# Kernel tuning notes

Measured on AMD Instinct MI355X. Metric: run time of the kernel, lower is better.

Reference implementation:

```python
import jax, jax.numpy as jnp
import numpy as np

D_MODEL = 1024
H = 16
D_K = D_MODEL // H
B = 128   # batch (intersample attention attends across this dim)
N = 256   # samples / tokens per row


def setup_inputs() -> dict:
    key = jax.random.key(0)
    ks = jax.random.split(key, 8)
    s = 1.0 / np.sqrt(D_MODEL)
    return {
        "query": jax.random.normal(ks[0], (B, N, D_MODEL), jnp.float32),
        "key":   jax.random.normal(ks[1], (B, N, D_MODEL), jnp.float32),
        "value": jax.random.normal(ks[2], (B, N, D_MODEL), jnp.float32),
        "Wq": jax.random.normal(ks[3], (D_MODEL, D_MODEL), jnp.float32) * s,
        "bq": jnp.zeros((D_MODEL,), jnp.float32),
        "Wk": jax.random.normal(ks[4], (D_MODEL, D_MODEL), jnp.float32) * s,
        "bk": jnp.zeros((D_MODEL,), jnp.float32),
        "Wv": jax.random.normal(ks[5], (D_MODEL, D_MODEL), jnp.float32) * s,
        "bv": jnp.zeros((D_MODEL,), jnp.float32),
        "Wo": jax.random.normal(ks[6], (D_MODEL, D_MODEL), jnp.float32) * s,
        "bo": jnp.zeros((D_MODEL,), jnp.float32),
    }


def _proj_heads(x, W, b):
    # torch nn.Linear: x @ W.T + b ; then view (b, n, h, d_k) -> (b, h, n, d_k)
    y = jnp.einsum('bnd,ed->bne', x, W) + b
    bsz, n, _ = y.shape
    return y.reshape(bsz, n, H, D_K).transpose(0, 2, 1, 3)


def reference(query, key, value, Wq, bq, Wk, bk, Wv, bv, Wo, bo):
    q = _proj_heads(query, Wq, bq)  # (b, h, n, d_k)
    k = _proj_heads(key,   Wk, bk)
    v = _proj_heads(value, Wv, bv)
    # intersample attention: attend ACROSS the batch dim b (per head, per sample n)
    scale = 1.0 / jnp.sqrt(jnp.asarray(D_K, q.dtype))
    scores = jnp.einsum('bhnd,chnd->hnbc', q, k) * scale  # (h, n, b, b)
    p = jax.nn.softmax(scores, axis=-1)
    out = jnp.einsum('hnbc,chnd->bhnd', p, v)             # (b, h, n, d_k)
    # merge heads: (b, h, n, d_k) -> (b, n, h*d_k)
    bsz, _, n, _ = out.shape
    out = out.transpose(0, 2, 1, 3).reshape(bsz, n, H * D_K)
    return jnp.einsum('bnd,ed->bne', out, Wo) + bo
```

## Files before the change

### kernel.cpp

```cpp
#include <hip/hip_runtime.h>
#include <hip/hip_bf16.h>
#include <stdint.h>

#define D_MODEL 1024
#define HEADS   16
#define DK      64
#define BATCH   128
#define NTOK    256
#define MROWS   (BATCH * NTOK)

typedef __attribute__((ext_vector_type(8))) short bf16x8;
typedef __attribute__((ext_vector_type(4))) float f32x4;

__device__ __forceinline__ unsigned short f2b_rne(float f) {
    union { float f; unsigned int u; } c; c.f = f;
    unsigned int u = c.u;
    unsigned int r = (u + 0x7FFFu + ((u >> 16) & 1u)) >> 16;
    return (unsigned short)r;
}

__device__ __forceinline__ void async16(const void* g, void* l) {
    __builtin_amdgcn_global_load_lds(
        (__attribute__((address_space(1))) void*)g,
        (__attribute__((address_space(3))) void*)l,
        16, 0, 0);
}

__global__ __launch_bounds__(256)
void f2b_kernel(const float* __restrict__ x, ushort* __restrict__ y, int n4) {
    int i = blockIdx.x * blockDim.x + threadIdx.x;
    int stride = gridDim.x * blockDim.x;
    for (; i < n4; i += stride) {
        float4 v = ((const float4*)x)[i];
        ushort4 o;
        o.x = f2b_rne(v.x); o.y = f2b_rne(v.y);
        o.z = f2b_rne(v.z); o.w = f2b_rne(v.w);
        ((ushort4*)y)[i] = o;
    }
}

template<int MODE>
__global__ __launch_bounds__(256)
void gemm_nt(const ushort* __restrict__ A, const ushort* __restrict__ B,
             const float* __restrict__ bias, void* __restrict__ Cout,
             int M, int N, int K, float alpha)
{
    __shared__ ushort As[128 * 32];
    __shared__ ushort Bs[128 * 32];

    const int tid  = threadIdx.x;
    const int wave = tid >> 6, lane = tid & 63;
    const int quad = lane >> 4, l15 = lane & 15;
    const int pm = blockIdx.x * 128, pn = blockIdx.y * 128;
    const int wm = (wave & 1) * 64, wn = (wave >> 1) * 64;

    f32x4 acc[4][4] = {};

    const int rg = lane >> 2;
    const int c8 = (lane & 3) * 8;
    const ushort* Abase0 = A + (size_t)(pm + wave * 32 + rg) * K + c8;
    const ushort* Abase1 = Abase0 + (size_t)16 * K;
    const ushort* Bbase0 = B + (size_t)(pn + wave * 32 + rg) * K + c8;
    const ushort* Bbase1 = Bbase0 + (size_t)16 * K;

    for (int k0 = 0; k0 < K; k0 += 32) {
        __syncthreads();
        async16(Abase0 + k0, &As[wave * 1024]);
        async16(Abase1 + k0, &As[wave * 1024 + 512]);
        async16(Bbase0 + k0, &Bs[wave * 1024]);
        async16(Bbase1 + k0, &Bs[wave * 1024 + 512]);
        __syncthreads();

        bf16x8 af[4], bfr[4];
        #pragma unroll
        for (int t = 0; t < 4; t++) {
            af[t]  = *(const bf16x8*)&As[(wm + t * 16 + l15) * 32 + quad * 8];
            bfr[t] = *(const bf16x8*)&Bs[(wn + t * 16 + l15) * 32 + quad * 8];
        }
        #pragma unroll
        for (int i = 0; i < 4; i++)
            #pragma unroll
            for (int j = 0; j < 4; j++)
                acc[i][j] = __builtin_amdgcn_mfma_f32_16x16x32_bf16(af[i], bfr[j], acc[i][j], 0, 0, 0);
    }

    if (MODE == 0) {
        ushort* out = (ushort*)Cout;
        #pragma unroll
        for (int i = 0; i < 4; i++) {
            const int mbase = pm + wm + i * 16 + quad * 4;
            #pragma unroll
            for (int j = 0; j < 4; j++) {
                const int e = pn + wn + j * 16 + l15;
                const float bv = bias[e];
                const int h = e >> 6, d = e & 63;
                #pragma unroll
                for (int r = 0; r < 4; r++) {
                    const int mm = mbase + r;
                    const int bb = mm >> 8, nn = mm & 255;
                    float val = (acc[i][j][r] + bv) * alpha;
                    out[(size_t)(((h << 8) + nn) * 128 + bb) * 64 + d] = f2b_rne(val);
                }
            }
        }
    } else {
        float* out = (float*)Cout;
        #pragma unroll
        for (int i = 0; i < 4; i++) {
            const int mbase = pm + wm + i * 16 + quad * 4;
            #pragma unroll
            for (int j = 0; j < 4; j++) {
                const int e = pn + wn + j * 16 + l15;
                const float bv = bias[e];
                #pragma unroll
                for (int r = 0; r < 4; r++) {
                    const int mm = mbase + r;
                    out[(size_t)mm * N + e] = acc[i][j][r] + bv;
                }
            }
        }
    }
}

__global__ __launch_bounds__(256)
void attn_kernel(const ushort* __restrict__ Qp, const ushort* __restrict__ Kp,
                 const ushort* __restrict__ Vp, ushort* __restrict__ Ob)
{
    __shared__ ushort sm[24576];

    const int tid  = threadIdx.x;
    const int wave = tid >> 6, lane = tid & 63;
    const int quad = lane >> 4, l15 = lane & 15;
    const int hn = blockIdx.x;
    const int h = hn >> 8, n = hn & 255;
    const size_t base = (size_t)hn * (BATCH * DK);

    {
        const uint4* Qg = (const uint4*)(Qp + base);
        const uint4* Kg = (const uint4*)(Kp + base);
        uint4* s4 = (uint4*)sm;
        #pragma unroll
        for (int i = 0; i < 4; i++) {
            int id = tid + i * 256;
            s4[id]        = Qg[id];
            s4[1024 + id] = Kg[id];
        }
        const uint4* Vg = (const uint4*)(Vp + base);
        #pragma unroll
        for (int i = 0; i < 4; i++) {
            int id = tid + i * 256;
            int c = id >> 3, d8 = (id & 7) * 8;
            uint4 vv = Vg[id];
            const ushort* vs = (const ushort*)&vv;
            #pragma unroll
            for (int j = 0; j < 8; j++)
                sm[16384 + (d8 + j) * 128 + c] = vs[j];
        }
    }
    __syncthreads();

    f32x4 accs[2][8] = {};
    #pragma unroll
    for (int kk = 0; kk < 64; kk += 32) {
        bf16x8 aq[2], bk8[8];
        #pragma unroll
        for (int mt = 0; mt < 2; mt++)
            aq[mt] = *(const bf16x8*)&sm[(wave * 32 + mt * 16 + l15) * 64 + kk + quad * 8];
        #pragma unroll
        for (int nt = 0; nt < 8; nt++)
            bk8[nt] = *(const bf16x8*)&sm[8192 + (nt * 16 + l15) * 64 + kk + quad * 8];
        #pragma unroll
        for (int mt = 0; mt < 2; mt++)
            #pragma unroll
            for (int nt = 0; nt < 8; nt++)
                accs[mt][nt] = __builtin_amdgcn_mfma_f32_16x16x32_bf16(aq[mt], bk8[nt], accs[mt][nt], 0, 0, 0);
    }

    #pragma unroll
    for (int mt = 0; mt < 2; mt++) {
        #pragma unroll
        for (int r = 0; r < 4; r++) {
            float mx = accs[mt][0][r];
            #pragma unroll
            for (int nt = 1; nt < 8; nt++) mx = fmaxf(mx, accs[mt][nt][r]);
            #pragma unroll
            for (int s = 1; s < 16; s <<= 1) mx = fmaxf(mx, __shfl_xor(mx, s, 64));
            float sum = 0.f;
            #pragma unroll
            for (int nt = 0; nt < 8; nt++) {
                float e = __expf(accs[mt][nt][r] - mx);
                accs[mt][nt][r] = e;
                sum += e;
            }
            #pragma unroll
            for (int s = 1; s < 16; s <<= 1) sum += __shfl_xor(sum, s, 64);
            float inv = 1.0f / sum;
            #pragma unroll
            for (int nt = 0; nt < 8; nt++) accs[mt][nt][r] *= inv;
        }
    }

    __syncthreads();

    #pragma unroll
    for (int mt = 0; mt < 2; mt++)
        #pragma unroll
        for (int nt = 0; nt < 8; nt++)
            #pragma unroll
            for (int r = 0; r < 4; r++)
                sm[(wave * 32 + mt * 16 + quad * 4 + r) * 128 + nt * 16 + l15] =
                    f2b_rne(accs[mt][nt][r]);
    __syncthreads();

    f32x4 acco[2][4] = {};
    #pragma unroll
    for (int kk = 0; kk < 128; kk += 32) {
        bf16x8 ap[2], bv8[4];
        #pragma unroll
        for (int mt = 0; mt < 2; mt++)
            ap[mt] = *(const bf16x8*)&sm[(wave * 32 + mt * 16 + l15) * 128 + kk + quad * 8];
        #pragma unroll
        for (int nt = 0; nt < 4; nt++)
            bv8[nt] = *(const bf16x8*)&sm[16384 + (nt * 16 + l15) * 128 + kk + quad * 8];
        #pragma unroll
        for (int mt = 0; mt < 2; mt++)
            #pragma unroll
            for (int nt = 0; nt < 4; nt++)
                acco[mt][nt] = __builtin_amdgcn_mfma_f32_16x16x32_bf16(ap[mt], bv8[nt], acco[mt][nt], 0, 0, 0);
    }

    #pragma unroll
    for (int mt = 0; mt < 2; mt++)
        #pragma unroll
        for (int nt = 0; nt < 4; nt++)
            #pragma unroll
            for (int r = 0; r < 4; r++) {
                int b = wave * 32 + mt * 16 + quad * 4 + r;
                int d = nt * 16 + l15;
                Ob[((size_t)b * NTOK + n) * D_MODEL + h * DK + d] = f2b_rne(acco[mt][nt][r]);
            }
}

extern "C" void kernel_launch(void* const* d_in, const int* in_sizes, int n_in,
                              void* d_out, int out_size, void* d_ws, size_t ws_size,
                              hipStream_t stream)
{
    const float* q  = (const float*)d_in[0];
    const float* k  = (const float*)d_in[1];
    const float* v  = (const float*)d_in[2];
    const float* Wq = (const float*)d_in[3];
    const float* bq = (const float*)d_in[4];
    const float* Wk = (const float*)d_in[5];
    const float* bk = (const float*)d_in[6];
    const float* Wv = (const float*)d_in[7];
    const float* bv = (const float*)d_in[8];
    const float* Wo = (const float*)d_in[9];
    const float* bo = (const float*)d_in[10];

    const int XE = MROWS * D_MODEL;
    const int WE = D_MODEL * D_MODEL;

    ushort* xb = (ushort*)d_ws;
    ushort* Kp = xb + (size_t)XE;
    ushort* Vp = Kp + (size_t)XE;
    ushort* Wb = Vp + (size_t)XE;
    ushort* Qp = (ushort*)d_out;

    dim3 blk(256);
    dim3 ggemm(MROWS / 128, D_MODEL / 128);

    f2b_kernel<<<dim3(512),  blk, 0, stream>>>(Wq, Wb + 0 * (size_t)WE, WE / 4);
    f2b_kernel<<<dim3(512),  blk, 0, stream>>>(Wk, Wb + 1 * (size_t)WE, WE / 4);
    f2b_kernel<<<dim3(512),  blk, 0, stream>>>(Wv, Wb + 2 * (size_t)WE, WE / 4);
    f2b_kernel<<<dim3(512),  blk, 0, stream>>>(Wo, Wb + 3 * (size_t)WE, WE / 4);

    f2b_kernel<<<dim3(4096), blk, 0, stream>>>(q, xb, XE / 4);
    gemm_nt<0><<<ggemm, blk, 0, stream>>>(xb, Wb + 0 * (size_t)WE, bq, Qp,
                                          MROWS, D_MODEL, D_MODEL, 0.125f);
    f2b_kernel<<<dim3(4096), blk, 0, stream>>>(k, xb, XE / 4);
    gemm_nt<0><<<ggemm, blk, 0, stream>>>(xb, Wb + 1 * (size_t)WE, bk, Kp,
                                          MROWS, D_MODEL, D_MODEL, 1.0f);
    f2b_kernel<<<dim3(4096), blk, 0, stream>>>(v, xb, XE / 4);
    gemm_nt<0><<<ggemm, blk, 0, stream>>>(xb, Wb + 2 * (size_t)WE, bv, Vp,
                                          MROWS, D_MODEL, D_MODEL, 1.0f);

    attn_kernel<<<dim3(HEADS * NTOK), blk, 0, stream>>>(Qp, Kp, Vp, xb);

    gemm_nt<1><<<ggemm, blk, 0, stream>>>(xb, Wb + 3 * (size_t)WE, bo, d_out,
                                          MROWS, D_MODEL, D_MODEL, 1.0f);
}
```

Measured before the change: 1.008 ms.

## Swizzle LDS layouts in GEMM and attention, fuse bf16 conversion launches

Rearranges the GEMM LDS tiles so each 16-row by 8-column fragment is stored contiguously, aiming to remove bank conflicts on the MFMA operand reads. The attention kernel gains XOR swizzles for the Q/K, transposed V and probability tiles in LDS for the same reason. Six separate fp32-to-bf16 conversion launches are merged into one kernel that converts q, k and all four weights. To make this possible, the buffer plan now places Vp in the output buffer after Qp and uses two input staging buffers, which assumes d_out has room for both.

```diff
diff --git a/kernel.cpp b/kernel.cpp
--- a/kernel.cpp
+++ b/kernel.cpp
@@ -39,14 +39,41 @@
     }
 }
 
+__global__ __launch_bounds__(256)
+void f2b6(const float* __restrict__ s0, ushort* __restrict__ d0, int n0,
+          const float* __restrict__ s1, ushort* __restrict__ d1, int n1,
+          const float* __restrict__ s2, ushort* __restrict__ d2, int n2,
+          const float* __restrict__ s3, ushort* __restrict__ d3, int n3,
+          const float* __restrict__ s4, ushort* __restrict__ d4, int n4c,
+          const float* __restrict__ s5, ushort* __restrict__ d5, int n5)
+{
+    int i = blockIdx.x * blockDim.x + threadIdx.x;
+    int stride = gridDim.x * blockDim.x;
+    const int t0 = n0, t1 = t0 + n1, t2 = t1 + n2, t3 = t2 + n3, t4 = t3 + n4c, t5 = t4 + n5;
+    for (; i < t5; i += stride) {
+        const float* s; ushort* d; int off;
+        if (i < t0)      { s = s0; d = d0; off = i; }
+        else if (i < t1) { s = s1; d = d1; off = i - t0; }
+        else if (i < t2) { s = s2; d = d2; off = i - t1; }
+        else if (i < t3) { s = s3; d = d3; off = i - t2; }
+        else if (i < t4) { s = s4; d = d4; off = i - t3; }
+        else             { s = s5; d = d5; off = i - t4; }
+        float4 v = ((const float4*)s)[off];
+        ushort4 o;
+        o.x = f2b_rne(v.x); o.y = f2b_rne(v.y);
+        o.z = f2b_rne(v.z); o.w = f2b_rne(v.w);
+        ((ushort4*)d)[off] = o;
+    }
+}
+
 template<int MODE>
 __global__ __launch_bounds__(256)
 void gemm_nt(const ushort* __restrict__ A, const ushort* __restrict__ B,
              const float* __restrict__ bias, void* __restrict__ Cout,
              int M, int N, int K, float alpha)
 {
-    __shared__ ushort As[128 * 32];
-    __shared__ ushort Bs[128 * 32];
+    __shared__ __align__(16) ushort As[128 * 32];
+    __shared__ __align__(16) ushort Bs[128 * 32];
 
     const int tid  = threadIdx.x;
     const int wave = tid >> 6, lane = tid & 63;
@@ -56,26 +83,26 @@
 
     f32x4 acc[4][4] = {};
 
-    const int rg = lane >> 2;
-    const int c8 = (lane & 3) * 8;
-    const ushort* Abase0 = A + (size_t)(pm + wave * 32 + rg) * K + c8;
+    const int r16 = lane & 15;
+    const int c8  = (lane >> 4) * 8;
+    const ushort* Abase0 = A + (size_t)(pm + wave * 32 + r16) * K + c8;
     const ushort* Abase1 = Abase0 + (size_t)16 * K;
-    const ushort* Bbase0 = B + (size_t)(pn + wave * 32 + rg) * K + c8;
+    const ushort* Bbase0 = B + (size_t)(pn + wave * 32 + r16) * K + c8;
     const ushort* Bbase1 = Bbase0 + (size_t)16 * K;
 
     for (int k0 = 0; k0 < K; k0 += 32) {
         __syncthreads();
-        async16(Abase0 + k0, &As[wave * 1024]);
-        async16(Abase1 + k0, &As[wave * 1024 + 512]);
-        async16(Bbase0 + k0, &Bs[wave * 1024]);
-        async16(Bbase1 + k0, &Bs[wave * 1024 + 512]);
+        async16(Abase0 + k0, &As[(wave * 2 + 0) * 512]);
+        async16(Abase1 + k0, &As[(wave * 2 + 1) * 512]);
+        async16(Bbase0 + k0, &Bs[(wave * 2 + 0) * 512]);
+        async16(Bbase1 + k0, &Bs[(wave * 2 + 1) * 512]);
         __syncthreads();
 
         bf16x8 af[4], bfr[4];
         #pragma unroll
         for (int t = 0; t < 4; t++) {
-            af[t]  = *(const bf16x8*)&As[(wm + t * 16 + l15) * 32 + quad * 8];
-            bfr[t] = *(const bf16x8*)&Bs[(wn + t * 16 + l15) * 32 + quad * 8];
+            af[t]  = *(const bf16x8*)&As[(((wave & 1) * 4 + t) * 4 + quad) * 128 + l15 * 8];
+            bfr[t] = *(const bf16x8*)&Bs[(((wave >> 1) * 4 + t) * 4 + quad) * 128 + l15 * 8];
         }
         #pragma unroll
         for (int i = 0; i < 4; i++)
@@ -126,14 +153,14 @@
 void attn_kernel(const ushort* __restrict__ Qp, const ushort* __restrict__ Kp,
                  const ushort* __restrict__ Vp, ushort* __restrict__ Ob)
 {
-    __shared__ ushort sm[24576];
+    __shared__ __align__(16) ushort sm[24576];
 
     const int tid  = threadIdx.x;
     const int wave = tid >> 6, lane = tid & 63;
     const int quad = lane >> 4, l15 = lane & 15;
     const int hn = blockIdx.x;
-    const int h = hn >> 8, n = hn & 255;
     const size_t base = (size_t)hn * (BATCH * DK);
+    const int n = hn & 255, h = hn >> 8;
 
     {
         const uint4* Qg = (const uint4*)(Qp + base);
@@ -142,19 +169,24 @@
         #pragma unroll
         for (int i = 0; i < 4; i++) {
             int id = tid + i * 256;
-            s4[id]        = Qg[id];
-            s4[1024 + id] = Kg[id];
+            int sw = (id & ~7) | ((id ^ (id >> 3)) & 7);
+            s4[sw]        = Qg[id];
+            s4[1024 + sw] = Kg[id];
         }
         const uint4* Vg = (const uint4*)(Vp + base);
         #pragma unroll
         for (int i = 0; i < 4; i++) {
             int id = tid + i * 256;
-            int c = id >> 3, d8 = (id & 7) * 8;
-            uint4 vv = Vg[id];
+            int c    = (id & 63) | ((id >> 9) << 6);
+            int dblk = (id >> 6) & 7;
+            uint4 vv = Vg[c * 8 + dblk];
             const ushort* vs = (const ushort*)&vv;
-            #pragma unroll
-            for (int j = 0; j < 8; j++)
-                sm[16384 + (d8 + j) * 128 + c] = vs[j];
+            int cb = c >> 3, cs = c & 7;
+            #pragma unroll
+            for (int j = 0; j < 8; j++) {
+                int d = dblk * 8 + j;
+                sm[16384 + d * 128 + ((cb ^ j) << 3) + cs] = vs[j];
+            }
         }
     }
     __syncthreads();
@@ -162,13 +194,15 @@
     f32x4 accs[2][8] = {};
     #pragma unroll
     for (int kk = 0; kk < 64; kk += 32) {
+        const int cbase = kk >> 3;
+        const int slot = ((cbase + quad) ^ (l15 & 7)) * 8;
         bf16x8 aq[2], bk8[8];
         #pragma unroll
         for (int mt = 0; mt < 2; mt++)
-            aq[mt] = *(const bf16x8*)&sm[(wave * 32 + mt * 16 + l15) * 64 + kk + quad * 8];
+            aq[mt] = *(const bf16x8*)&sm[(wave * 32 + mt * 16 + l15) * 64 + slot];
         #pragma unroll
         for (int nt = 0; nt < 8; nt++)
-            bk8[nt] = *(const bf16x8*)&sm[8192 + (nt * 16 + l15) * 64 + kk + quad * 8];
+            bk8[nt] = *(const bf16x8*)&sm[8192 + (nt * 16 + l15) * 64 + slot];
         #pragma unroll
         for (int mt = 0; mt < 2; mt++)
             #pragma unroll
@@ -203,25 +237,32 @@
     __syncthreads();
 
     #pragma unroll
-    for (int mt = 0; mt < 2; mt++)
-        #pragma unroll
-        for (int nt = 0; nt < 8; nt++)
-            #pragma unroll
-            for (int r = 0; r < 4; r++)
-                sm[(wave * 32 + mt * 16 + quad * 4 + r) * 128 + nt * 16 + l15] =
-                    f2b_rne(accs[mt][nt][r]);
+    for (int mt = 0; mt < 2; mt++) {
+        #pragma unroll
+        for (int r = 0; r < 4; r++) {
+            const int row = wave * 32 + mt * 16 + quad * 4 + r;
+            const int rs = row & 7;
+            #pragma unroll
+            for (int nt = 0; nt < 8; nt++) {
+                int chunk = nt * 2 + (l15 >> 3);
+                sm[row * 128 + ((chunk ^ rs) << 3) + (l15 & 7)] = f2b_rne(accs[mt][nt][r]);
+            }
+        }
+    }
     __syncthreads();
 
     f32x4 acco[2][4] = {};
     #pragma unroll
     for (int kk = 0; kk < 128; kk += 32) {
+        const int cbase = kk >> 3;
+        const int slot = (((cbase + quad) ^ (l15 & 7)) & 15) * 8;
         bf16x8 ap[2], bv8[4];
         #pragma unroll
         for (int mt = 0; mt < 2; mt++)
-            ap[mt] = *(const bf16x8*)&sm[(wave * 32 + mt * 16 + l15) * 128 + kk + quad * 8];
+            ap[mt] = *(const bf16x8*)&sm[(wave * 32 + mt * 16 + l15) * 128 + slot];
         #pragma unroll
         for (int nt = 0; nt < 4; nt++)
-            bv8[nt] = *(const bf16x8*)&sm[16384 + (nt * 16 + l15) * 128 + kk + quad * 8];
+            bv8[nt] = *(const bf16x8*)&sm[16384 + (nt * 16 + l15) * 128 + slot];
         #pragma unroll
         for (int mt = 0; mt < 2; mt++)
             #pragma unroll
@@ -260,32 +301,35 @@
     const int XE = MROWS * D_MODEL;
     const int WE = D_MODEL * D_MODEL;
 
-    ushort* xb = (ushort*)d_ws;
-    ushort* Kp = xb + (size_t)XE;
-    ushort* Vp = Kp + (size_t)XE;
-    ushort* Wb = Vp + (size_t)XE;
+    ushort* xb1 = (ushort*)d_ws;
+    ushort* xb2 = xb1 + (size_t)XE;
+    ushort* Kp  = xb2 + (size_t)XE;
+    ushort* Wb  = Kp  + (size_t)XE;
     ushort* Qp = (ushort*)d_out;
+    ushort* Vp = Qp + (size_t)XE;
 
     dim3 blk(256);
     dim3 ggemm(MROWS / 128, D_MODEL / 128);
 
-    f2b_kernel<<<dim3(512),  blk, 0, stream>>>(Wq, Wb + 0 * (size_t)WE, WE / 4);
-    f2b_kernel<<<dim3(512),  blk, 0, stream>>>(Wk, Wb + 1 * (size_t)WE, WE / 4);
-    f2b_kernel<<<dim3(512),  blk, 0, stream>>>(Wv, Wb + 2 * (size_t)WE, WE / 4);
-    f2b_kernel<<<dim3(512),  blk, 0, stream>>>(Wo, Wb + 3 * (size_t)WE, WE / 4);
-
-    f2b_kernel<<<dim3(4096), blk, 0, stream>>>(q, xb, XE / 4);
-    gemm_nt<0><<<ggemm, blk, 0, stream>>>(xb, Wb + 0 * (size_t)WE, bq, Qp,
+    f2b6<<<dim3(4096), blk, 0, stream>>>(
+        q,  xb1,              XE / 4,
+        k,  xb2,              XE / 4,
+        Wq, Wb + 0 * (size_t)WE, WE / 4,
+        Wk, Wb + 1 * (size_t)WE, WE / 4,
+        Wv, Wb + 2 * (size_t)WE, WE / 4,
+        Wo, Wb + 3 * (size_t)WE, WE / 4);
+
+    gemm_nt<0><<<ggemm, blk, 0, stream>>>(xb1, Wb + 0 * (size_t)WE, bq, Qp,
                                           MROWS, D_MODEL, D_MODEL, 0.125f);
-    f2b_kernel<<<dim3(4096), blk, 0, stream>>>(k, xb, XE / 4);
-    gemm_nt<0><<<ggemm, blk, 0, stream>>>(xb, Wb + 1 * (size_t)WE, bk, Kp,
+    gemm_nt<0><<<ggemm, blk, 0, stream>>>(xb2, Wb + 1 * (size_t)WE, bk, Kp,
                                           MROWS, D_MODEL, D_MODEL, 1.0f);
-    f2b_kernel<<<dim3(4096), blk, 0, stream>>>(v, xb, XE / 4);
-    gemm_nt<0><<<ggemm, blk, 0, stream>>>(xb, Wb + 2 * (size_t)WE, bv, Vp,
+
+    f2b_kernel<<<dim3(4096), blk, 0, stream>>>(v, xb2, XE / 4);
+    gemm_nt<0><<<ggemm, blk, 0, stream>>>(xb2, Wb + 2 * (size_t)WE, bv, Vp,
                                           MROWS, D_MODEL, D_MODEL, 1.0f);
 
-    attn_kernel<<<dim3(HEADS * NTOK), blk, 0, stream>>>(Qp, Kp, Vp, xb);
-
-    gemm_nt<1><<<ggemm, blk, 0, stream>>>(xb, Wb + 3 * (size_t)WE, bo, d_out,
+    attn_kernel<<<dim3(HEADS * NTOK), blk, 0, stream>>>(Qp, Kp, Vp, xb1);
+
+    gemm_nt<1><<<ggemm, blk, 0, stream>>>(xb1, Wb + 3 * (size_t)WE, bo, d_out,
                                           MROWS, D_MODEL, D_MODEL, 1.0f);
 }
```

After: 1.122 ms. +11.3%, slower.
